# Kernel optimization log

Hardware: AMD Instinct MI355X
Metric: run time of the kernel (lower is better)

## Reference

```python
import jax, jax.numpy as jnp
import numpy as np

N_NODES = 50000
N_EDGES = 400000
IN_DIM = 128
HIDDEN = 128
OUT_DIM = 128
MIX = 4

def _gelu(x):
    return jax.nn.gelu(x, approximate=False)  # torch default erf-GELU

def setup_inputs() -> dict:
    key = jax.random.key(0)
    ks = jax.random.split(key, 8)
    X = jax.random.normal(ks[0], (N_NODES, IN_DIM), dtype=jnp.float32)
    edge_index = jax.random.randint(ks[1], (2, N_EDGES), 0, N_NODES, dtype=jnp.int64)
    s = lambda fan_in: 1.0 / np.sqrt(fan_in)
    W1 = jax.random.uniform(ks[2], (HIDDEN, IN_DIM), jnp.float32, -s(IN_DIM), s(IN_DIM))
    b1 = jax.random.uniform(ks[3], (HIDDEN,), jnp.float32, -s(IN_DIM), s(IN_DIM))
    WA = jax.random.uniform(ks[4], (HIDDEN, HIDDEN), jnp.float32, -s(HIDDEN), s(HIDDEN))
    WB = jax.random.uniform(ks[5], (MIX, HIDDEN), jnp.float32, -s(HIDDEN), s(HIDDEN))
    W2 = jax.random.uniform(ks[6], (OUT_DIM, 2 * HIDDEN), jnp.float32, -s(2 * HIDDEN), s(2 * HIDDEN))
    b2 = jax.random.uniform(ks[7], (OUT_DIM,), jnp.float32, -s(2 * HIDDEN), s(2 * HIDDEN))
    return {"X": X, "edge_index": edge_index, "W1": W1, "b1": b1,
            "WA": WA, "WB": WB, "W2": W2, "b2": b2}

def reference(X, edge_index, W1, b1, WA, WB, W2, b2):
    num_nodes = X.shape[0]
    # ff1 -> gelu (dropout identity in eval)
    H = _gelu(X @ W1.T + b1)                       # (N, h)
    src, dst = edge_index[0], edge_index[1]
    X_src = H[src]                                 # (E, h) gather
    # hyper target weights per edge
    W_tar = _gelu(X_src @ WA.T) @ WB.T             # (E, m)
    # per-edge outer product, scatter_add over dst
    cross = X_src[:, :, None] * W_tar[:, None, :]  # (E, h, m)
    agg = jax.ops.segment_sum(cross, dst, num_segments=num_nodes)  # (N, h, m)
    agg = _gelu(agg)
    # gather back per edge, contract mix dim
    out_edge = jnp.einsum('ehm,em->eh', agg[dst], W_tar)  # (E, h)
    # scatter_mean over dst
    ones = jnp.ones((src.shape[0],), X.dtype)
    cnt = jax.ops.segment_sum(ones, dst, num_segments=num_nodes)   # (N,)
    agg_node = jax.ops.segment_sum(out_edge, dst, num_segments=num_nodes)
    agg_node = agg_node / jnp.maximum(cnt, 1.0)[:, None]           # (N, h)
    # root connection + gelu, ff2
    feat = _gelu(jnp.concatenate([agg_node, H], axis=1))           # (N, 2h)
    out = feat @ W2.T + b2                                          # (N, out)
    return out
```

## Files before the change

kernel.cpp:

```cpp
#include <hip/hip_runtime.h>
#include <hip/hip_bf16.h>

#define NN 50000
#define NE 400000
#define NT 3125

typedef unsigned short u16;
typedef short short8 __attribute__((ext_vector_type(8)));
typedef float f32x4 __attribute__((ext_vector_type(4)));

__device__ __forceinline__ float geluf(float x){ return 0.5f*x*(1.0f+erff(x*0.70710678118654752440f)); }
__device__ __forceinline__ u16 f2bfb(float f){
  union { __hip_bfloat16 h; u16 u; } cv; cv.h = __float2bfloat16(f); return cv.u;
}
__device__ __forceinline__ float bfb2f(u16 u){ return __uint_as_float(((unsigned)u)<<16); }

__global__ __launch_bounds__(256) void k_pre(const float* __restrict__ W1,
    const float* __restrict__ WA, const float* __restrict__ W2,
    u16* __restrict__ W1b, u16* __restrict__ WAb, u16* __restrict__ W2b,
    const int* __restrict__ dst, int* __restrict__ deg)
{
  if (blockIdx.x < 64){
    int i4 = (blockIdx.x*256 + threadIdx.x) * 4;
    const float* srcp; u16* dstp; int off;
    if (i4 < 16384){ srcp = W1; dstp = W1b; off = i4; }
    else if (i4 < 32768){ srcp = WA; dstp = WAb; off = i4 - 16384; }
    else { srcp = W2; dstp = W2b; off = i4 - 32768; }
    float4 v = *(const float4*)(srcp + off);
    ushort4 o;
    o.x = f2bfb(v.x); o.y = f2bfb(v.y); o.z = f2bfb(v.z); o.w = f2bfb(v.w);
    *(ushort4*)(dstp + off) = o;
  } else {
    int e = (blockIdx.x - 64)*256 + threadIdx.x;
    if (e < NE) atomicAdd(&deg[dst[e]], 1);
  }
}

__global__ __launch_bounds__(512) void k_ff1(const float* __restrict__ X,
    const u16* __restrict__ W1b, const float* __restrict__ b1,
    u16* __restrict__ Hb)
{
  extern __shared__ u16 wls[];
  const int LDW = 136;
  for (int idx8 = threadIdx.x*8; idx8 < 128*128; idx8 += 512*8){
    int c = idx8 >> 7, k = idx8 & 127;
    *(short8*)&wls[c*LDW + k] = *(const short8*)(W1b + idx8);
  }
  __syncthreads();
  const int lane = threadIdx.x & 63;
  const int wave = threadIdx.x >> 6;
  const int lrow = lane & 15;
  const int kgrp = lane >> 4;
  float4 b1v[8];
  #pragma unroll
  for (int nb = 0; nb < 8; nb++) b1v[nb] = *(const float4*)(b1 + nb*16 + kgrp*4);
  for (int tile = wave*gridDim.x + blockIdx.x; tile < NT; tile += gridDim.x*8){
    const float* xr = X + (size_t)(tile*16 + lrow)*128 + kgrp*8;
    f32x4 acc[8];
    #pragma unroll
    for (int nb = 0; nb < 8; nb++) acc[nb] = (f32x4){0.f,0.f,0.f,0.f};
    #pragma unroll
    for (int kk = 0; kk < 4; kk++){
      float4 xa = *(const float4*)(xr + kk*32);
      float4 xb = *(const float4*)(xr + kk*32 + 4);
      union { short8 v; u16 u[8]; } af;
      af.u[0]=f2bfb(xa.x); af.u[1]=f2bfb(xa.y); af.u[2]=f2bfb(xa.z); af.u[3]=f2bfb(xa.w);
      af.u[4]=f2bfb(xb.x); af.u[5]=f2bfb(xb.y); af.u[6]=f2bfb(xb.z); af.u[7]=f2bfb(xb.w);
      #pragma unroll
      for (int nb = 0; nb < 8; nb++){
        short8 bf = *(const short8*)&wls[(nb*16 + lrow)*LDW + kk*32 + kgrp*8];
        acc[nb] = __builtin_amdgcn_mfma_f32_16x16x32_bf16(bf, af.v, acc[nb], 0, 0, 0);
      }
    }
    const size_t rb = (size_t)(tile*16 + lrow)*128 + kgrp*4;
    #pragma unroll
    for (int nb = 0; nb < 8; nb++){
      ushort4 hp;
      #pragma unroll
      for (int r = 0; r < 4; r++)
        ((u16*)&hp)[r] = f2bfb(geluf(acc[nb][r] + b1v[nb][r]));
      *(ushort4*)(Hb + rb + nb*16) = hp;
    }
  }
}

__global__ __launch_bounds__(1024) void k_scan(const int* __restrict__ deg, int* __restrict__ offs){
  __shared__ int wsum[16];
  __shared__ int sbase_s;
  const int tid = threadIdx.x, lane = tid & 63, wave = tid >> 6;
  if (tid == 0) sbase_s = 0;
  __syncthreads();
  for (int base = 0; base < NN; base += 4096){
    int i0 = base + tid*4;
    int v0=0,v1=0,v2=0,v3=0;
    if (i0+3 < NN){ int4 v = *(const int4*)(deg+i0); v0=v.x;v1=v.y;v2=v.z;v3=v.w; }
    else {
      if (i0   < NN) v0 = deg[i0];
      if (i0+1 < NN) v1 = deg[i0+1];
      if (i0+2 < NN) v2 = deg[i0+2];
    }
    int own = v0+v1+v2+v3;
    int inc = own;
    #pragma unroll
    for (int s=1;s<64;s<<=1){ int t = __shfl_up(inc, s, 64); if (lane >= s) inc += t; }
    if (lane == 63) wsum[wave] = inc;
    __syncthreads();
    if (wave == 0 && lane < 16){
      int w = wsum[lane];
      #pragma unroll
      for (int s=1;s<16;s<<=1){ int t = __shfl_up(w, s, 64); if (lane >= s) w += t; }
      wsum[lane] = w;
    }
    __syncthreads();
    int sbase = sbase_s;
    int wbase = sbase + (wave ? wsum[wave-1] : 0);
    int excl = wbase + inc - own;
    if (i0   < NN) offs[i0]   = excl;
    if (i0+1 < NN) offs[i0+1] = excl + v0;
    if (i0+2 < NN) offs[i0+2] = excl + v0+v1;
    if (i0+3 < NN) offs[i0+3] = excl + v0+v1+v2;
    __syncthreads();
    if (tid == 0) sbase_s = sbase + wsum[15];
    __syncthreads();
  }
  if (tid == 0) offs[NN] = sbase_s;
}

__global__ void k_fill(const int* __restrict__ src, const int* __restrict__ dst,
                       const int* __restrict__ offs, int* __restrict__ cur,
                       int* __restrict__ slist){
  int e = blockIdx.x*256 + threadIdx.x;
  if (e < NE){
    int d = dst[e];
    int p = atomicAdd(&cur[d], 1);
    slist[offs[d] + p] = src[e];
  }
}

__global__ __launch_bounds__(512) void k_node(const u16* __restrict__ Hb,
    const u16* __restrict__ WAb, const float* __restrict__ WB,
    float* __restrict__ T)
{
  extern __shared__ u16 was[];
  const int LDW = 136;
  for (int idx8 = threadIdx.x*8; idx8 < 128*128; idx8 += 512*8){
    int h = idx8 >> 7, k = idx8 & 127;
    *(short8*)&was[h*LDW + k] = *(const short8*)(WAb + idx8);
  }
  const int lane = threadIdx.x & 63;
  const int wave = threadIdx.x >> 6;
  const int lrow = lane & 15;
  const int kgrp = lane >> 4;
  float wbv[4][8];
  #pragma unroll
  for (int m = 0; m < 4; m++)
    #pragma unroll
    for (int nb = 0; nb < 8; nb++)
      wbv[m][nb] = WB[m*128 + nb*16 + lrow];
  __syncthreads();
  for (int tile = wave*gridDim.x + blockIdx.x; tile < NT; tile += gridDim.x*8){
    const u16* hr = Hb + (size_t)(tile*16 + lrow)*128 + kgrp*8;
    f32x4 acc[8];
    #pragma unroll
    for (int nb = 0; nb < 8; nb++) acc[nb] = (f32x4){0.f,0.f,0.f,0.f};
    #pragma unroll
    for (int kk = 0; kk < 4; kk++){
      short8 af = *(const short8*)(hr + kk*32);
      #pragma unroll
      for (int nb = 0; nb < 8; nb++){
        short8 bf = *(const short8*)&was[(nb*16 + lrow)*LDW + kk*32 + kgrp*8];
        acc[nb] = __builtin_amdgcn_mfma_f32_16x16x32_bf16(af, bf, acc[nb], 0, 0, 0);
      }
    }
    float part[4][4];
    #pragma unroll
    for (int r = 0; r < 4; r++)
      #pragma unroll
      for (int m = 0; m < 4; m++) part[r][m] = 0.f;
    #pragma unroll
    for (int nb = 0; nb < 8; nb++){
      float g0 = geluf(acc[nb][0]), g1 = geluf(acc[nb][1]);
      float g2 = geluf(acc[nb][2]), g3 = geluf(acc[nb][3]);
      #pragma unroll
      for (int m = 0; m < 4; m++){
        float w = wbv[m][nb];
        part[0][m] += g0*w; part[1][m] += g1*w;
        part[2][m] += g2*w; part[3][m] += g3*w;
      }
    }
    #pragma unroll
    for (int s = 1; s < 16; s <<= 1)
      #pragma unroll
      for (int r = 0; r < 4; r++)
        #pragma unroll
        for (int m = 0; m < 4; m++)
          part[r][m] += __shfl_xor(part[r][m], s, 64);
    if (lrow == 0){
      #pragma unroll
      for (int r = 0; r < 4; r++){
        f32x4 tv = { part[r][0], part[r][1], part[r][2], part[r][3] };
        *(f32x4*)&T[(size_t)(tile*16 + kgrp*4 + r)*4] = tv;
      }
    }
  }
}

__global__ __launch_bounds__(256) void k_agg(const u16* __restrict__ Hb,
    const float* __restrict__ T, const int* __restrict__ offs,
    const int* __restrict__ slist, u16* __restrict__ GAb)
{
  const int lane = threadIdx.x & 63;
  const int wave = threadIdx.x >> 6;
  const int vo = lane*2;
  for (int v = blockIdx.x*4 + wave; v < NN; v += gridDim.x*4){
    const int e0 = __builtin_amdgcn_readfirstlane(offs[v]);
    const int e1 = __builtin_amdgcn_readfirstlane(offs[v+1]);
    float ax0=0, ax1=0, ax2=0, ax3=0;
    float ay0=0, ay1=0, ay2=0, ay3=0;
    float s0=0, s1=0, s2=0, s3=0;
    int idx = e0;
    for (; idx + 8 <= e1; idx += 8){
      unsigned pk[8]; float4 tt[8];
      #pragma unroll
      for (int u = 0; u < 8; u++){
        int sn = slist[idx+u];
        pk[u] = *(const unsigned*)(Hb + (size_t)sn*128 + vo);
        tt[u] = *(const float4*)(T + (size_t)sn*4);
      }
      #pragma unroll
      for (int u = 0; u < 8; u++){
        float hx = bfb2f((u16)(pk[u] & 0xffffu));
        float hy = bfb2f((u16)(pk[u] >> 16));
        ax0 += hx*tt[u].x; ax1 += hx*tt[u].y; ax2 += hx*tt[u].z; ax3 += hx*tt[u].w;
        ay0 += hy*tt[u].x; ay1 += hy*tt[u].y; ay2 += hy*tt[u].z; ay3 += hy*tt[u].w;
        s0 += tt[u].x; s1 += tt[u].y; s2 += tt[u].z; s3 += tt[u].w;
      }
    }
    for (; idx + 4 <= e1; idx += 4){
      unsigned pk[4]; float4 tt[4];
      #pragma unroll
      for (int u = 0; u < 4; u++){
        int sn = slist[idx+u];
        pk[u] = *(const unsigned*)(Hb + (size_t)sn*128 + vo);
        tt[u] = *(const float4*)(T + (size_t)sn*4);
      }
      #pragma unroll
      for (int u = 0; u < 4; u++){
        float hx = bfb2f((u16)(pk[u] & 0xffffu));
        float hy = bfb2f((u16)(pk[u] >> 16));
        ax0 += hx*tt[u].x; ax1 += hx*tt[u].y; ax2 += hx*tt[u].z; ax3 += hx*tt[u].w;
        ay0 += hy*tt[u].x; ay1 += hy*tt[u].y; ay2 += hy*tt[u].z; ay3 += hy*tt[u].w;
        s0 += tt[u].x; s1 += tt[u].y; s2 += tt[u].z; s3 += tt[u].w;
      }
    }
    for (; idx < e1; idx++){
      int sn = slist[idx];
      unsigned pk = *(const unsigned*)(Hb + (size_t)sn*128 + vo);
      float hx = bfb2f((u16)(pk & 0xffffu));
      float hy = bfb2f((u16)(pk >> 16));
      float4 wt = *(const float4*)(T + (size_t)sn*4);
      ax0 += hx*wt.x; ax1 += hx*wt.y; ax2 += hx*wt.z; ax3 += hx*wt.w;
      ay0 += hy*wt.x; ay1 += hy*wt.y; ay2 += hy*wt.z; ay3 += hy*wt.w;
      s0 += wt.x; s1 += wt.y; s2 += wt.z; s3 += wt.w;
    }
    float inv = 1.0f / fmaxf((float)(e1 - e0), 1.0f);
    float ox = geluf(ax0)*s0 + geluf(ax1)*s1 + geluf(ax2)*s2 + geluf(ax3)*s3;
    float oy = geluf(ay0)*s0 + geluf(ay1)*s1 + geluf(ay2)*s2 + geluf(ay3)*s3;
    ushort2 res;
    res.x = f2bfb(geluf(ox * inv));
    res.y = f2bfb(geluf(oy * inv));
    *(ushort2*)(GAb + (size_t)v*128 + vo) = res;
  }
}

__global__ __launch_bounds__(512) void k_ff2(const u16* __restrict__ GAb,
    const u16* __restrict__ Hb, const u16* __restrict__ W2b,
    const float* __restrict__ b2, float* __restrict__ out)
{
  extern __shared__ u16 w2s[];
  const int LDW = 264;
  for (int idx8 = threadIdx.x*8; idx8 < 128*256; idx8 += 512*8){
    int o = idx8 >> 8, k = idx8 & 255;
    *(short8*)&w2s[o*LDW + k] = *(const short8*)(W2b + idx8);
  }
  __syncthreads();
  const int lane = threadIdx.x & 63;
  const int wave = threadIdx.x >> 6;
  const int lrow = lane & 15;
  const int kgrp = lane >> 4;
  float4 b2v[8];
  #pragma unroll
  for (int nb = 0; nb < 8; nb++) b2v[nb] = *(const float4*)(b2 + nb*16 + kgrp*4);
  for (int tile = wave*gridDim.x + blockIdx.x; tile < NT; tile += gridDim.x*8){
    const int row = tile*16 + lrow;
    const u16* aga = GAb + (size_t)row*128 + kgrp*8;
    const u16* agh = Hb  + (size_t)row*128 + kgrp*8;
    f32x4 acc[8];
    #pragma unroll
    for (int nb = 0; nb < 8; nb++) acc[nb] = (f32x4){0.f,0.f,0.f,0.f};
    #pragma unroll
    for (int kk = 0; kk < 8; kk++){
      short8 af;
      if (kk < 4){
        af = *(const short8*)(aga + kk*32);
      } else {
        short8 hb = *(const short8*)(agh + (kk-4)*32);
        union { short8 v; u16 u[8]; } g;
        #pragma unroll
        for (int j = 0; j < 8; j++)
          g.u[j] = f2bfb(geluf(bfb2f(((const u16*)&hb)[j])));
        af = g.v;
      }
      #pragma unroll
      for (int nb = 0; nb < 8; nb++){
        short8 bf = *(const short8*)&w2s[(nb*16 + lrow)*LDW + kk*32 + kgrp*8];
        acc[nb] = __builtin_amdgcn_mfma_f32_16x16x32_bf16(bf, af, acc[nb], 0, 0, 0);
      }
    }
    float* orp = out + (size_t)row*128 + kgrp*4;
    #pragma unroll
    for (int nb = 0; nb < 8; nb++){
      f32x4 o;
      o[0] = acc[nb][0] + b2v[nb].x;
      o[1] = acc[nb][1] + b2v[nb].y;
      o[2] = acc[nb][2] + b2v[nb].z;
      o[3] = acc[nb][3] + b2v[nb].w;
      *(f32x4*)(orp + nb*16) = o;
    }
  }
}

extern "C" void kernel_launch(void* const* d_in, const int* in_sizes, int n_in,
                              void* d_out, int out_size, void* d_ws, size_t ws_size,
                              hipStream_t stream)
{
  (void)in_sizes; (void)n_in; (void)out_size; (void)ws_size;
  const float* X  = (const float*)d_in[0];
  const int*   ei = (const int*)d_in[1];
  const float* W1 = (const float*)d_in[2];
  const float* b1 = (const float*)d_in[3];
  const float* WA = (const float*)d_in[4];
  const float* WB = (const float*)d_in[5];
  const float* W2 = (const float*)d_in[6];
  const float* b2 = (const float*)d_in[7];
  float* out = (float*)d_out;
  const int* src = ei;
  const int* dst = ei + NE;

  char* p = (char*)d_ws;
  u16*   Hb   = (u16*)(p);
  u16*   GAb  = (u16*)(p + 12800000);
  float* T    = (float*)(p + 25600000);
  int*   deg  = (int*)(p + 26400000);
  int*   cur  = (int*)(p + 26600192);
  int*   offs = (int*)(p + 26800384);
  int*   slist= (int*)(p + 27000832);
  u16*   W1b  = (u16*)(p + 28600832);
  u16*   WAb  = (u16*)(p + 28633600);
  u16*   W2b  = (u16*)(p + 28666368);

  (void)hipMemsetAsync(deg, 0, 400384, stream);

  (void)hipFuncSetAttribute((const void*)k_ff2, hipFuncAttributeMaxDynamicSharedMemorySize, 128*264*2);

  k_pre <<<64 + (NE+255)/256, 256, 0, stream>>>(W1, WA, W2, W1b, WAb, W2b, dst, deg);
  k_ff1 <<<512, 512, 128*136*2, stream>>>(X, W1b, b1, Hb);
  k_scan<<<1, 1024, 0, stream>>>(deg, offs);
  k_fill<<<(NE+255)/256, 256, 0, stream>>>(src, dst, offs, cur, slist);
  k_node<<<512, 512, 128*136*2, stream>>>(Hb, WAb, WB, T);
  k_agg <<<2048, 256, 0, stream>>>(Hb, T, offs, slist, GAb);
  k_ff2 <<<512, 512, 128*264*2, stream>>>(GAb, Hb, W2b, b2, out);
}
```

Measured before the change: 171.7 us.

## Fuse node hyper-weight GEMM into ff1 kernel via LDS-staged H tile

Merges the per-node WA GEMM, GELU and WB projection into the ff1 kernel. Each wave stages its freshly computed bf16 H tile in LDS and immediately runs the second MFMA pass, so the separate launch and the global re-read of H are gone. Tile assignment changes to block-contiguous, and the grids for ff1n and ff2 shrink to 391 blocks. LDS per block rises to about 102 KB, which may limit occupancy to one block per CU.

```diff
diff --git a/kernel.cpp b/kernel.cpp
--- a/kernel.cpp
+++ b/kernel.cpp
@@ -36,25 +36,36 @@
   }
 }
 
-__global__ __launch_bounds__(512) void k_ff1(const float* __restrict__ X,
+__global__ __launch_bounds__(512) void k_ff1n(const float* __restrict__ X,
     const u16* __restrict__ W1b, const float* __restrict__ b1,
-    u16* __restrict__ Hb)
-{
-  extern __shared__ u16 wls[];
+    const u16* __restrict__ WAb, const float* __restrict__ WB,
+    u16* __restrict__ Hb, float* __restrict__ T)
+{
+  extern __shared__ u16 smem[];
+  u16* w1s = smem;
+  u16* was = smem + 17408;
   const int LDW = 136;
   for (int idx8 = threadIdx.x*8; idx8 < 128*128; idx8 += 512*8){
     int c = idx8 >> 7, k = idx8 & 127;
-    *(short8*)&wls[c*LDW + k] = *(const short8*)(W1b + idx8);
+    *(short8*)&w1s[c*LDW + k] = *(const short8*)(W1b + idx8);
+    *(short8*)&was[c*LDW + k] = *(const short8*)(WAb + idx8);
   }
   __syncthreads();
   const int lane = threadIdx.x & 63;
   const int wave = threadIdx.x >> 6;
   const int lrow = lane & 15;
   const int kgrp = lane >> 4;
+  u16* hls = smem + 34816 + wave*(16*LDW);
   float4 b1v[8];
   #pragma unroll
   for (int nb = 0; nb < 8; nb++) b1v[nb] = *(const float4*)(b1 + nb*16 + kgrp*4);
-  for (int tile = wave*gridDim.x + blockIdx.x; tile < NT; tile += gridDim.x*8){
+  float wbv[4][8];
+  #pragma unroll
+  for (int m = 0; m < 4; m++)
+    #pragma unroll
+    for (int nb = 0; nb < 8; nb++)
+      wbv[m][nb] = WB[m*128 + nb*16 + lrow];
+  for (int tile = blockIdx.x*8 + wave; tile < NT; tile += gridDim.x*8){
     const float* xr = X + (size_t)(tile*16 + lrow)*128 + kgrp*8;
     f32x4 acc[8];
     #pragma unroll
@@ -68,7 +79,7 @@
       af.u[4]=f2bfb(xb.x); af.u[5]=f2bfb(xb.y); af.u[6]=f2bfb(xb.z); af.u[7]=f2bfb(xb.w);
       #pragma unroll
       for (int nb = 0; nb < 8; nb++){
-        short8 bf = *(const short8*)&wls[(nb*16 + lrow)*LDW + kk*32 + kgrp*8];
+        short8 bf = *(const short8*)&w1s[(nb*16 + lrow)*LDW + kk*32 + kgrp*8];
         acc[nb] = __builtin_amdgcn_mfma_f32_16x16x32_bf16(bf, af.v, acc[nb], 0, 0, 0);
       }
     }
@@ -80,6 +91,49 @@
       for (int r = 0; r < 4; r++)
         ((u16*)&hp)[r] = f2bfb(geluf(acc[nb][r] + b1v[nb][r]));
       *(ushort4*)(Hb + rb + nb*16) = hp;
+      *(ushort4*)&hls[lrow*LDW + nb*16 + kgrp*4] = hp;
+    }
+    f32x4 acc2[8];
+    #pragma unroll
+    for (int nb = 0; nb < 8; nb++) acc2[nb] = (f32x4){0.f,0.f,0.f,0.f};
+    #pragma unroll
+    for (int kk = 0; kk < 4; kk++){
+      short8 af = *(const short8*)&hls[lrow*LDW + kk*32 + kgrp*8];
+      #pragma unroll
+      for (int nb = 0; nb < 8; nb++){
+        short8 bf = *(const short8*)&was[(nb*16 + lrow)*LDW + kk*32 + kgrp*8];
+        acc2[nb] = __builtin_amdgcn_mfma_f32_16x16x32_bf16(af, bf, acc2[nb], 0, 0, 0);
+      }
+    }
+    float part[4][4];
+    #pragma unroll
+    for (int r = 0; r < 4; r++)
+      #pragma unroll
+      for (int m = 0; m < 4; m++) part[r][m] = 0.f;
+    #pragma unroll
+    for (int nb = 0; nb < 8; nb++){
+      float g0 = geluf(acc2[nb][0]), g1 = geluf(acc2[nb][1]);
+      float g2 = geluf(acc2[nb][2]), g3 = geluf(acc2[nb][3]);
+      #pragma unroll
+      for (int m = 0; m < 4; m++){
+        float w = wbv[m][nb];
+        part[0][m] += g0*w; part[1][m] += g1*w;
+        part[2][m] += g2*w; part[3][m] += g3*w;
+      }
+    }
+    #pragma unroll
+    for (int s = 1; s < 16; s <<= 1)
+      #pragma unroll
+      for (int r = 0; r < 4; r++)
+        #pragma unroll
+        for (int m = 0; m < 4; m++)
+          part[r][m] += __shfl_xor(part[r][m], s, 64);
+    if (lrow == 0){
+      #pragma unroll
+      for (int r = 0; r < 4; r++){
+        f32x4 tv = { part[r][0], part[r][1], part[r][2], part[r][3] };
+        *(f32x4*)&T[(size_t)(tile*16 + kgrp*4 + r)*4] = tv;
+      }
     }
   }
 }
@@ -137,74 +191,6 @@
   }
 }
 
-__global__ __launch_bounds__(512) void k_node(const u16* __restrict__ Hb,
-    const u16* __restrict__ WAb, const float* __restrict__ WB,
-    float* __restrict__ T)
-{
-  extern __shared__ u16 was[];
-  const int LDW = 136;
-  for (int idx8 = threadIdx.x*8; idx8 < 128*128; idx8 += 512*8){
-    int h = idx8 >> 7, k = idx8 & 127;
-    *(short8*)&was[h*LDW + k] = *(const short8*)(WAb + idx8);
-  }
-  const int lane = threadIdx.x & 63;
-  const int wave = threadIdx.x >> 6;
-  const int lrow = lane & 15;
-  const int kgrp = lane >> 4;
-  float wbv[4][8];
-  #pragma unroll
-  for (int m = 0; m < 4; m++)
-    #pragma unroll
-    for (int nb = 0; nb < 8; nb++)
-      wbv[m][nb] = WB[m*128 + nb*16 + lrow];
-  __syncthreads();
-  for (int tile = wave*gridDim.x + blockIdx.x; tile < NT; tile += gridDim.x*8){
-    const u16* hr = Hb + (size_t)(tile*16 + lrow)*128 + kgrp*8;
-    f32x4 acc[8];
-    #pragma unroll
-    for (int nb = 0; nb < 8; nb++) acc[nb] = (f32x4){0.f,0.f,0.f,0.f};
-    #pragma unroll
-    for (int kk = 0; kk < 4; kk++){
-      short8 af = *(const short8*)(hr + kk*32);
-      #pragma unroll
-      for (int nb = 0; nb < 8; nb++){
-        short8 bf = *(const short8*)&was[(nb*16 + lrow)*LDW + kk*32 + kgrp*8];
-        acc[nb] = __builtin_amdgcn_mfma_f32_16x16x32_bf16(af, bf, acc[nb], 0, 0, 0);
-      }
-    }
-    float part[4][4];
-    #pragma unroll
-    for (int r = 0; r < 4; r++)
-      #pragma unroll
-      for (int m = 0; m < 4; m++) part[r][m] = 0.f;
-    #pragma unroll
-    for (int nb = 0; nb < 8; nb++){
-      float g0 = geluf(acc[nb][0]), g1 = geluf(acc[nb][1]);
-      float g2 = geluf(acc[nb][2]), g3 = geluf(acc[nb][3]);
-      #pragma unroll
-      for (int m = 0; m < 4; m++){
-        float w = wbv[m][nb];
-        part[0][m] += g0*w; part[1][m] += g1*w;
-        part[2][m] += g2*w; part[3][m] += g3*w;
-      }
-    }
-    #pragma unroll
-    for (int s = 1; s < 16; s <<= 1)
-      #pragma unroll
-      for (int r = 0; r < 4; r++)
-        #pragma unroll
-        for (int m = 0; m < 4; m++)
-          part[r][m] += __shfl_xor(part[r][m], s, 64);
-    if (lrow == 0){
-      #pragma unroll
-      for (int r = 0; r < 4; r++){
-        f32x4 tv = { part[r][0], part[r][1], part[r][2], part[r][3] };
-        *(f32x4*)&T[(size_t)(tile*16 + kgrp*4 + r)*4] = tv;
-      }
-    }
-  }
-}
-
 __global__ __launch_bounds__(256) void k_agg(const u16* __restrict__ Hb,
     const float* __restrict__ T, const int* __restrict__ offs,
     const int* __restrict__ slist, u16* __restrict__ GAb)
@@ -291,7 +277,7 @@
   float4 b2v[8];
   #pragma unroll
   for (int nb = 0; nb < 8; nb++) b2v[nb] = *(const float4*)(b2 + nb*16 + kgrp*4);
-  for (int tile = wave*gridDim.x + blockIdx.x; tile < NT; tile += gridDim.x*8){
+  for (int tile = blockIdx.x*8 + wave; tile < NT; tile += gridDim.x*8){
     const int row = tile*16 + lrow;
     const u16* aga = GAb + (size_t)row*128 + kgrp*8;
     const u16* agh = Hb  + (size_t)row*128 + kgrp*8;
@@ -361,13 +347,13 @@
 
   (void)hipMemsetAsync(deg, 0, 400384, stream);
 
-  (void)hipFuncSetAttribute((const void*)k_ff2, hipFuncAttributeMaxDynamicSharedMemorySize, 128*264*2);
+  (void)hipFuncSetAttribute((const void*)k_ff1n, hipFuncAttributeMaxDynamicSharedMemorySize, 104448);
+  (void)hipFuncSetAttribute((const void*)k_ff2,  hipFuncAttributeMaxDynamicSharedMemorySize, 128*264*2);
 
   k_pre <<<64 + (NE+255)/256, 256, 0, stream>>>(W1, WA, W2, W1b, WAb, W2b, dst, deg);
-  k_ff1 <<<512, 512, 128*136*2, stream>>>(X, W1b, b1, Hb);
+  k_ff1n<<<391, 512, 104448, stream>>>(X, W1b, b1, WAb, WB, Hb, T);
   k_scan<<<1, 1024, 0, stream>>>(deg, offs);
   k_fill<<<(NE+255)/256, 256, 0, stream>>>(src, dst, offs, cur, slist);
-  k_node<<<512, 512, 128*136*2, stream>>>(Hb, WAb, WB, T);
   k_agg <<<2048, 256, 0, stream>>>(Hb, T, offs, slist, GAb);
-  k_ff2 <<<512, 512, 128*264*2, stream>>>(GAb, Hb, W2b, b2, out);
-}
+  k_ff2 <<<391, 512, 128*264*2, stream>>>(GAb, Hb, W2b, b2, out);
+}
```

Measured after the change: 166.3 us. -3.1%, faster.
